# Performance work log

Measured on AMD Instinct MI355X. Metric: run time of the kernel, lower is better.

The kernel has to match this reference:

```python
import jax, jax.numpy as jnp
import numpy as np

HIDDEN = 64

def setup_inputs() -> dict:
    key = jax.random.key(0)
    ks = jax.random.split(key, 7)
    B, T, I, H, O = 4096, 512, 28, 64, 10
    s_ih = 1.0 / np.sqrt(H)
    return {
        "x": jax.random.normal(ks[0], (B, T, I), dtype=jnp.float32),
        "W_ih": jax.random.uniform(ks[1], (H, I), jnp.float32, -s_ih, s_ih),
        "W_hh": jax.random.uniform(ks[2], (H, H), jnp.float32, -s_ih, s_ih),
        "b_ih": jax.random.uniform(ks[3], (H,), jnp.float32, -s_ih, s_ih),
        "b_hh": jax.random.uniform(ks[4], (H,), jnp.float32, -s_ih, s_ih),
        "W_out": jax.random.uniform(ks[5], (O, H), jnp.float32, -s_ih, s_ih),
        "b_out": jax.random.uniform(ks[6], (O,), jnp.float32, -s_ih, s_ih),
    }

def reference(x, W_ih, W_hh, b_ih, b_hh, W_out, b_out):
    B, T, I = x.shape
    # Precompute input contributions for all timesteps: [T, B, H]
    xW = jnp.einsum('bti,hi->tbh', x, W_ih) + b_ih + b_hh
    h0 = jnp.zeros((B, HIDDEN), dtype=x.dtype)

    def step(h, xw_t):
        h_new = jnp.tanh(xw_t + h @ W_hh.T)
        return h_new, None

    h_last, _ = jax.lax.scan(step, h0, xW)
    return h_last @ W_out.T + b_out
```

## Files before the change

### kernel.cpp

```cpp
#include <hip/hip_runtime.h>


#define T_STEPS 512
#define I_DIM   28
#define H_DIM   64
#define O_DIM   10
#define ROWS    16

#define RS_EL   72
#define LO_EL   1152
#define LO_FR   144
#define BUF_EL  2304
#define BUF_FR  288

typedef __attribute__((ext_vector_type(8))) short bfrag;
typedef __attribute__((ext_vector_type(4))) float ffrag;
typedef __attribute__((ext_vector_type(4))) float float4v;

#define MFMA(a,b,c) __builtin_amdgcn_mfma_f32_16x16x32_bf16((a),(b),(c),0,0,0)
#define LDS_BARRIER() asm volatile("s_waitcnt lgkmcnt(0)\n\ts_barrier" ::: "memory")

union FragU { bfrag s; unsigned u[4]; };

__device__ __forceinline__ unsigned hi_pack(float f0, float f1){
  return __builtin_amdgcn_perm(__float_as_uint(f1), __float_as_uint(f0), 0x07060302u);
}

__device__ __forceinline__ void split8v(float4v a, float4v b, bfrag& hi, bfrag& lo){
  float f[8] = {a.x,a.y,a.z,a.w, b.x,b.y,b.z,b.w};
  FragU H, L;
#pragma unroll
  for (int m = 0; m < 4; m++){
    float f0 = f[2*m], f1 = f[2*m+1];
    H.u[m] = hi_pack(f0, f1);
    float l0 = f0 - __uint_as_float(__float_as_uint(f0) & 0xffff0000u);
    float l1 = f1 - __uint_as_float(__float_as_uint(f1) & 0xffff0000u);
    L.u[m] = hi_pack(l0, l1);
  }
  hi = H.s; lo = L.s;
}

__device__ __forceinline__ float fast_tanh(float p){
  float e = __builtin_amdgcn_exp2f(p * 2.88539008177792681f);
  return __builtin_fmaf(-2.0f, __builtin_amdgcn_rcpf(e + 1.0f), 1.0f);
}

#define BODY(K, WP, RP, PF)                                                    \
  {                                                                            \
    bfrag xhi, xlo;                                                            \
    split8v(xa[K], xb[K], xhi, xlo);                                           \
    if (PF){                                                                   \
      xa[K] = *(const float4v*)(xpa + ((K) + 4) * I_DIM);                      \
      xb[K] = *(const float4v*)(xpb + ((K) + 4) * I_DIM);                      \
    }                                                                          \
    ffrag P, Q, R;                                                             \
                    \
    P = MFMA(xhi, wih_hi, biasf);                                              \
    Q = MFMA(xhi, wih_lo, zfrag);                                              \
    P = MFMA(xlo, wih_hi, P);                                                  \
                             \
    P = MFMA(h_hi[0], whh_hi[0], P);                                           \
    Q = MFMA(h_hi[1], whh_hi[1], Q);                                           \
    R = MFMA(h_hi[0], whh_lo[0], zfrag);                                       \
    P = MFMA(h_lo[0], whh_hi[0], P);                                           \
    Q = MFMA(h_lo[1], whh_hi[1], Q);                                           \
    R = MFMA(h_hi[1], whh_lo[1], R);                                           \
    float fs[4];                                                               \
    fs[0] = (P.x + Q.x) + R.x;                                                 \
    fs[1] = (P.y + Q.y) + R.y;                                                 \
    fs[2] = (P.z + Q.z) + R.z;                                                 \
    fs[3] = (P.w + Q.w) + R.w;                                                 \
         \
    _Pragma("unroll")                                                          \
    for (int m = 0; m < 4; ++m){                                               \
      float f = fast_tanh(fs[m]);                                              \
      unsigned u = __float_as_uint(f);                                         \
      (WP)[m*RS_EL] = (unsigned short)(u >> 16);                               \
      float l = f - __uint_as_float(u & 0xffff0000u);                          \
      (WP)[m*RS_EL + LO_EL] = (unsigned short)(__float_as_uint(l) >> 16);      \
    }                                                                          \
    LDS_BARRIER();                                                             \
     \
    h_hi[0] = (RP)[0];                                                         \
    h_hi[1] = (RP)[4];                                                         \
    h_lo[0] = (RP)[LO_FR];                                                     \
    h_lo[1] = (RP)[LO_FR + 4];                                                 \
  }

__global__ __launch_bounds__(256, 1) void rnn_fused(
    const float* __restrict__ x,
    const float* __restrict__ W_ih,
    const float* __restrict__ W_hh,
    const float* __restrict__ b_ih,
    const float* __restrict__ b_hh,
    const float* __restrict__ W_out,
    const float* __restrict__ b_out,
    float* __restrict__ out)
{
  __shared__ bfrag hsv[2 * BUF_FR];
  const int tid  = threadIdx.x;
  const int w    = tid >> 6;
  const int lane = tid & 63;
  const int c    = lane & 15;
  const int q    = lane >> 4;
  const bool qlt3 = (q < 3);
  const int rowbase = blockIdx.x * ROWS;

  bfrag whh_hi[2], whh_lo[2];
#pragma unroll
  for (int kt = 0; kt < 2; ++kt){
    const float* p = W_hh + (c + 16*w)*H_DIM + kt*32 + q*8;
    split8v(*(const float4v*)p, *(const float4v*)(p + 4), whh_hi[kt], whh_lo[kt]);
  }

  bfrag wih_hi, wih_lo;
  {
    const float* p = W_ih + (c + 16*w)*I_DIM + q*8;
    float4v a = *(const float4v*)p;
    float4v b;
    if (qlt3) b = *(const float4v*)(p + 4);
    else      b = (float4v){0.f, 0.f, 0.f, 0.f};
    split8v(a, b, wih_hi, wih_lo);
  }

  ffrag biasf;
  {
    float bb = b_ih[c + 16*w] + b_hh[c + 16*w];
    biasf.x = bb; biasf.y = bb; biasf.z = bb; biasf.w = bb;
  }
  const ffrag zfrag = {0.f, 0.f, 0.f, 0.f};

  bfrag h_hi[2], h_lo[2];
  {
    FragU Z; Z.u[0]=Z.u[1]=Z.u[2]=Z.u[3]=0;
    h_hi[0] = Z.s; h_lo[0] = Z.s; h_hi[1] = Z.s; h_lo[1] = Z.s;
  }

  unsigned short* const wbase = (unsigned short*)hsv;
  unsigned short* const wp0 = wbase + 0*BUF_EL + (4*q)*RS_EL + (c + 16*w);
  unsigned short* const wp1 = wbase + 1*BUF_EL + (4*q)*RS_EL + (c + 16*w);
  const bfrag* const rp0 = hsv + 0*BUF_FR + 9*c + q;
  const bfrag* const rp1 = hsv + 1*BUF_FR + 9*c + q;

  const float* xpa = x + ((size_t)(rowbase + c) * T_STEPS) * I_DIM + q*8;
  const float* xpb = qlt3 ? xpa + 4 : xpa;
  float4v xa[4], xb[4];
#pragma unroll
  for (int s = 0; s < 4; ++s){
    xa[s] = *(const float4v*)(xpa + s * I_DIM);
    xb[s] = *(const float4v*)(xpb + s * I_DIM);
  }

#pragma unroll 1
  for (int tb = 0; tb < T_STEPS - 4; tb += 4){
    BODY(0, wp1, rp1, 1)
    BODY(1, wp0, rp0, 1)
    BODY(2, wp1, rp1, 1)
    BODY(3, wp0, rp0, 1)
    xpa += 4 * I_DIM;
    xpb += 4 * I_DIM;
  }
  BODY(0, wp1, rp1, 0)
  BODY(1, wp0, rp0, 0)
  BODY(2, wp1, rp1, 0)
  BODY(3, wp0, rp0, 0)

  if (w == 0){
    const unsigned short* hb = (const unsigned short*)hsv;
    for (int oo = q; oo < O_DIM; oo += 4){
      float s = b_out[oo];
#pragma unroll 8
      for (int k = 0; k < H_DIM; ++k){
        float hv = __uint_as_float((unsigned)hb[c*RS_EL + k] << 16)
                 + __uint_as_float((unsigned)hb[c*RS_EL + k + LO_EL] << 16);
        s += hv * W_out[oo*H_DIM + k];
      }
      out[(size_t)(rowbase + c)*O_DIM + oo] = s;
    }
  }
}

extern "C" void kernel_launch(void* const* d_in, const int* in_sizes, int n_in,
                              void* d_out, int out_size, void* d_ws, size_t ws_size,
                              hipStream_t stream) {
  const float* x     = (const float*)d_in[0];
  const float* W_ih  = (const float*)d_in[1];
  const float* W_hh  = (const float*)d_in[2];
  const float* b_ih  = (const float*)d_in[3];
  const float* b_hh  = (const float*)d_in[4];
  const float* W_out = (const float*)d_in[5];
  const float* b_out = (const float*)d_in[6];
  float* out = (float*)d_out;

  int B = in_sizes[0] / (T_STEPS * I_DIM);
  rnn_fused<<<B / ROWS, 256, 0, stream>>>(x, W_ih, W_hh, b_ih, b_hh, W_out, b_out, out);
}
```

Baseline: 442.6 us.

## Add producer warps that stage split bf16 x fragments through LDS

Doubles the block to 512 threads. Four new producer waves load x from global memory, split it into bf16 hi/lo fragments and write them into an 8-slot LDS ring. The four compute waves read each step's input fragment from LDS and no longer do global loads or the split inside the recurrence. This takes global-load latency and the split ALU work off the serial critical path, at the cost of more LDS traffic, a tightly coupled barrier count between producer and consumer waves, and more waves per block.

After: 395.8 us. 10.6% less time.

```diff
diff --git a/kernel.cpp b/kernel.cpp
--- a/kernel.cpp
+++ b/kernel.cpp
@@ -12,6 +12,7 @@
 #define LO_FR   144
 #define BUF_EL  2304
 #define BUF_FR  288
+#define XSLOT_FR 64
 
 typedef __attribute__((ext_vector_type(8))) short bfrag;
 typedef __attribute__((ext_vector_type(4))) float ffrag;
@@ -45,16 +46,11 @@
   return __builtin_fmaf(-2.0f, __builtin_amdgcn_rcpf(e + 1.0f), 1.0f);
 }
 
-#define BODY(K, WP, RP, PF)                                                    \
+#define BODY_C(WP, RP, NS)                                                     \
   {                                                                            \
-    bfrag xhi, xlo;                                                            \
-    split8v(xa[K], xb[K], xhi, xlo);                                           \
-    if (PF){                                                                   \
-      xa[K] = *(const float4v*)(xpa + ((K) + 4) * I_DIM);                      \
-      xb[K] = *(const float4v*)(xpb + ((K) + 4) * I_DIM);                      \
-    }                                                                          \
+    bfrag xhi = nxh, xlo = nxl;                                                \
     ffrag P, Q, R;                                                             \
-                    \
+           \
     P = MFMA(xhi, wih_hi, biasf);                                              \
     Q = MFMA(xhi, wih_lo, zfrag);                                              \
     P = MFMA(xlo, wih_hi, P);                                                  \
@@ -79,15 +75,26 @@
       float l = f - __uint_as_float(u & 0xffff0000u);                          \
       (WP)[m*RS_EL + LO_EL] = (unsigned short)(__float_as_uint(l) >> 16);      \
     }                                                                          \
+                  \
+    nxh = xrh[(NS) * XSLOT_FR];                                                \
+    nxl = xrl[(NS) * XSLOT_FR];                                                \
     LDS_BARRIER();                                                             \
-     \
+      \
     h_hi[0] = (RP)[0];                                                         \
     h_hi[1] = (RP)[4];                                                         \
     h_lo[0] = (RP)[LO_FR];                                                     \
     h_lo[1] = (RP)[LO_FR + 4];                                                 \
   }
 
-__global__ __launch_bounds__(256, 1) void rnn_fused(
+#define PRODUCE(AR, BR, S)                                                     \
+  {                                                                            \
+    bfrag fh, fl;                                                              \
+    split8v(AR, BR, fh, fl);                                                   \
+    xwh[(S) * XSLOT_FR] = fh;                                                  \
+    xwl[(S) * XSLOT_FR] = fl;                                                  \
+  }
+
+__global__ __launch_bounds__(512, 1) void rnn_fused(
     const float* __restrict__ x,
     const float* __restrict__ W_ih,
     const float* __restrict__ W_hh,
@@ -98,6 +105,8 @@
     float* __restrict__ out)
 {
   __shared__ bfrag hsv[2 * BUF_FR];
+  __shared__ bfrag xhi_s[8 * XSLOT_FR];
+  __shared__ bfrag xlo_s[8 * XSLOT_FR];
   const int tid  = threadIdx.x;
   const int w    = tid >> 6;
   const int lane = tid & 63;
@@ -106,77 +115,118 @@
   const bool qlt3 = (q < 3);
   const int rowbase = blockIdx.x * ROWS;
 
-  bfrag whh_hi[2], whh_lo[2];
+  if (w < 4){
+    bfrag whh_hi[2], whh_lo[2];
 #pragma unroll
-  for (int kt = 0; kt < 2; ++kt){
-    const float* p = W_hh + (c + 16*w)*H_DIM + kt*32 + q*8;
-    split8v(*(const float4v*)p, *(const float4v*)(p + 4), whh_hi[kt], whh_lo[kt]);
-  }
-
-  bfrag wih_hi, wih_lo;
-  {
-    const float* p = W_ih + (c + 16*w)*I_DIM + q*8;
-    float4v a = *(const float4v*)p;
-    float4v b;
-    if (qlt3) b = *(const float4v*)(p + 4);
-    else      b = (float4v){0.f, 0.f, 0.f, 0.f};
-    split8v(a, b, wih_hi, wih_lo);
-  }
-
-  ffrag biasf;
-  {
-    float bb = b_ih[c + 16*w] + b_hh[c + 16*w];
-    biasf.x = bb; biasf.y = bb; biasf.z = bb; biasf.w = bb;
-  }
-  const ffrag zfrag = {0.f, 0.f, 0.f, 0.f};
-
-  bfrag h_hi[2], h_lo[2];
-  {
-    FragU Z; Z.u[0]=Z.u[1]=Z.u[2]=Z.u[3]=0;
-    h_hi[0] = Z.s; h_lo[0] = Z.s; h_hi[1] = Z.s; h_lo[1] = Z.s;
-  }
-
-  unsigned short* const wbase = (unsigned short*)hsv;
-  unsigned short* const wp0 = wbase + 0*BUF_EL + (4*q)*RS_EL + (c + 16*w);
-  unsigned short* const wp1 = wbase + 1*BUF_EL + (4*q)*RS_EL + (c + 16*w);
-  const bfrag* const rp0 = hsv + 0*BUF_FR + 9*c + q;
-  const bfrag* const rp1 = hsv + 1*BUF_FR + 9*c + q;
-
-  const float* xpa = x + ((size_t)(rowbase + c) * T_STEPS) * I_DIM + q*8;
-  const float* xpb = qlt3 ? xpa + 4 : xpa;
-  float4v xa[4], xb[4];
-#pragma unroll
-  for (int s = 0; s < 4; ++s){
-    xa[s] = *(const float4v*)(xpa + s * I_DIM);
-    xb[s] = *(const float4v*)(xpb + s * I_DIM);
-  }
+    for (int kt = 0; kt < 2; ++kt){
+      const float* p = W_hh + (c + 16*w)*H_DIM + kt*32 + q*8;
+      split8v(*(const float4v*)p, *(const float4v*)(p + 4), whh_hi[kt], whh_lo[kt]);
+    }
+
+    bfrag wih_hi, wih_lo;
+    {
+      const float* p = W_ih + (c + 16*w)*I_DIM + q*8;
+      float4v a = *(const float4v*)p;
+      float4v b;
+      if (qlt3) b = *(const float4v*)(p + 4);
+      else      b = (float4v){0.f, 0.f, 0.f, 0.f};
+      split8v(a, b, wih_hi, wih_lo);
+    }
+
+    ffrag biasf;
+    {
+      float bb = b_ih[c + 16*w] + b_hh[c + 16*w];
+      biasf.x = bb; biasf.y = bb; biasf.z = bb; biasf.w = bb;
+    }
+    const ffrag zfrag = {0.f, 0.f, 0.f, 0.f};
+
+    bfrag h_hi[2], h_lo[2];
+    {
+      FragU Z; Z.u[0]=Z.u[1]=Z.u[2]=Z.u[3]=0;
+      h_hi[0] = Z.s; h_lo[0] = Z.s; h_hi[1] = Z.s; h_lo[1] = Z.s;
+    }
+
+    unsigned short* const wbase = (unsigned short*)hsv;
+    unsigned short* const wp0 = wbase + 0*BUF_EL + (4*q)*RS_EL + (c + 16*w);
+    unsigned short* const wp1 = wbase + 1*BUF_EL + (4*q)*RS_EL + (c + 16*w);
+    const bfrag* const rp0 = hsv + 0*BUF_FR + 9*c + q;
+    const bfrag* const rp1 = hsv + 1*BUF_FR + 9*c + q;
+    const bfrag* const xrh = xhi_s + lane;
+    const bfrag* const xrl = xlo_s + lane;
+
+    LDS_BARRIER();
+    bfrag nxh = xrh[0], nxl = xrl[0];
 
 #pragma unroll 1
-  for (int tb = 0; tb < T_STEPS - 4; tb += 4){
-    BODY(0, wp1, rp1, 1)
-    BODY(1, wp0, rp0, 1)
-    BODY(2, wp1, rp1, 1)
-    BODY(3, wp0, rp0, 1)
-    xpa += 4 * I_DIM;
-    xpb += 4 * I_DIM;
-  }
-  BODY(0, wp1, rp1, 0)
-  BODY(1, wp0, rp0, 0)
-  BODY(2, wp1, rp1, 0)
-  BODY(3, wp0, rp0, 0)
-
-  if (w == 0){
-    const unsigned short* hb = (const unsigned short*)hsv;
-    for (int oo = q; oo < O_DIM; oo += 4){
-      float s = b_out[oo];
+    for (int j = 0; j < 63; ++j){
+      BODY_C(wp1, rp1, 1)
+      BODY_C(wp0, rp0, 2)
+      BODY_C(wp1, rp1, 3)
+      BODY_C(wp0, rp0, 4)
+      BODY_C(wp1, rp1, 5)
+      BODY_C(wp0, rp0, 6)
+      BODY_C(wp1, rp1, 7)
+      BODY_C(wp0, rp0, 0)
+    }
+    BODY_C(wp1, rp1, 1)
+    BODY_C(wp0, rp0, 2)
+    BODY_C(wp1, rp1, 3)
+    BODY_C(wp0, rp0, 4)
+    BODY_C(wp1, rp1, 5)
+    BODY_C(wp0, rp0, 6)
+    BODY_C(wp1, rp1, 7)
+    BODY_C(wp0, rp0, 0)
+
+    if (w == 0){
+      const unsigned short* hb = (const unsigned short*)hsv;
+      for (int oo = q; oo < O_DIM; oo += 4){
+        float s = b_out[oo];
 #pragma unroll 8
-      for (int k = 0; k < H_DIM; ++k){
-        float hv = __uint_as_float((unsigned)hb[c*RS_EL + k] << 16)
-                 + __uint_as_float((unsigned)hb[c*RS_EL + k + LO_EL] << 16);
-        s += hv * W_out[oo*H_DIM + k];
+        for (int k = 0; k < H_DIM; ++k){
+          float hv = __uint_as_float((unsigned)hb[c*RS_EL + k] << 16)
+                   + __uint_as_float((unsigned)hb[c*RS_EL + k + LO_EL] << 16);
+          s += hv * W_out[oo*H_DIM + k];
+        }
+        out[(size_t)(rowbase + c)*O_DIM + oo] = s;
       }
-      out[(size_t)(rowbase + c)*O_DIM + oo] = s;
-    }
+    }
+  } else {
+    const int p = w - 4;
+    const float* xpa = x + ((size_t)(rowbase + c) * T_STEPS) * I_DIM + q*8;
+    const float* xpb = qlt3 ? xpa + 4 : xpa;
+    bfrag* const xwh = xhi_s + lane;
+    bfrag* const xwl = xlo_s + lane;
+
+    float4v a0 = *(const float4v*)(xpa + p*I_DIM);
+    float4v b0 = *(const float4v*)(xpb + p*I_DIM);
+    float4v aA = *(const float4v*)(xpa + (4+p)*I_DIM);
+    float4v bA = *(const float4v*)(xpb + (4+p)*I_DIM);
+    float4v aB = *(const float4v*)(xpa + (8+p)*I_DIM);
+    float4v bB = *(const float4v*)(xpb + (8+p)*I_DIM);
+    PRODUCE(a0, b0, p)
+    LDS_BARRIER();
+
+    const float* la = xpa + (size_t)(12+p)*I_DIM;
+    const float* lb = xpb + (size_t)(12+p)*I_DIM;
+#pragma unroll 1
+    for (int j = 0; j < 63; ++j){
+      PRODUCE(aA, bA, 4 + p)
+      aA = *(const float4v*)la;
+      bA = *(const float4v*)lb;
+      LDS_BARRIER(); LDS_BARRIER(); LDS_BARRIER(); LDS_BARRIER();
+      PRODUCE(aB, bB, p)
+      {
+        const float* ca = (j < 62) ? la + 4*I_DIM : la;
+        const float* cb = (j < 62) ? lb + 4*I_DIM : lb;
+        aB = *(const float4v*)ca;
+        bB = *(const float4v*)cb;
+      }
+      la += 8*I_DIM; lb += 8*I_DIM;
+      LDS_BARRIER(); LDS_BARRIER(); LDS_BARRIER(); LDS_BARRIER();
+    }
+    PRODUCE(aA, bA, 4 + p)
+    LDS_BARRIER(); LDS_BARRIER(); LDS_BARRIER(); LDS_BARRIER();
+    LDS_BARRIER(); LDS_BARRIER(); LDS_BARRIER(); LDS_BARRIER();
   }
 }
 
@@ -193,5 +243,5 @@
   float* out = (float*)d_out;
 
   int B = in_sizes[0] / (T_STEPS * I_DIM);
-  rnn_fused<<<B / ROWS, 256, 0, stream>>>(x, W_ih, W_hh, b_ih, b_hh, W_out, b_out, out);
-}
+  rnn_fused<<<B / ROWS, 512, 0, stream>>>(x, W_ih, W_hh, b_ih, b_hh, W_out, b_out, out);
+}
```
